# Performance work log

Measured on AMD Instinct MI355X. Metric: run time of the kernel, lower is better.

## Reference

```python
import jax, jax.numpy as jnp
import numpy as np

B, S, H, NH = 2, 2048, 1024, 16
HD = H // NH
EPS = 1e-6

def rotate_half(x):
    x1, x2 = jnp.split(x, 2, axis=-1)
    return jnp.concatenate([-x2, x1], axis=-1)

def setup_inputs() -> dict:
    key = jax.random.key(0)
    ks = jax.random.split(key, 4)
    x = jax.random.normal(ks[0], (B, S, H), dtype=jnp.float32)
    # rotary angles
    inv_freq = 1.0 / (10000.0 ** (np.arange(0, HD, 2, dtype=np.float32) / HD))
    t = np.arange(S, dtype=np.float32)
    freqs = np.einsum('s,d->sd', t, inv_freq)
    emb = np.concatenate([freqs, freqs], axis=-1)  # [S, HD]
    cos = jnp.broadcast_to(jnp.cos(emb)[None], (B, S, HD)).astype(jnp.float32)
    sin = jnp.broadcast_to(jnp.sin(emb)[None], (B, S, HD)).astype(jnp.float32)
    attn_mask = jnp.broadcast_to(jnp.tril(jnp.ones((S, S), jnp.float32))[None], (B, S, S))
    W_uvqk = jax.random.normal(ks[1], (4 * H, H), dtype=jnp.float32) * (1.0 / np.sqrt(H))
    b_uvqk = jnp.zeros((4 * H,), jnp.float32)
    gate_w = jnp.ones((H,), jnp.float32)
    W_out = jax.random.normal(ks[2], (H, H), dtype=jnp.float32) * (1.0 / np.sqrt(H))
    b_out = jnp.zeros((H,), jnp.float32)
    return {"x": x, "cos": cos, "sin": sin, "attn_mask": attn_mask,
            "W_uvqk": W_uvqk, "b_uvqk": b_uvqk, "gate_w": gate_w,
            "W_out": W_out, "b_out": b_out}

def reference(x, cos, sin, attn_mask, W_uvqk, b_uvqk, gate_w, W_out, b_out):
    b, s, h = x.shape
    residual = x
    uvqk = jnp.einsum('bsh,oh->bso', x, W_uvqk) + b_uvqk
    u, v, q, k = jnp.split(uvqk, 4, axis=-1)
    u = jax.nn.silu(u)
    q = q.reshape(b, s, NH, HD)
    k = k.reshape(b, s, NH, HD)
    v = v.reshape(b, s, NH, HD)
    c = cos[:, :, None, :]  # [B,S,1,HD] broadcasts over heads
    sn = sin[:, :, None, :]
    q = q * c + rotate_half(q) * sn
    k = k * c + rotate_half(k) * sn
    # [B,NH,S,S] raw scores -> silu (no softmax) -> mask -> AV
    scores = jnp.einsum('bqnd,bknd->bnqk', q, k) / np.sqrt(HD).astype(np.float32)
    attn = jax.nn.silu(scores) * attn_mask[:, None, :, :]
    attn_out = jnp.einsum('bnqk,bknd->bqnd', attn, v).reshape(b, s, h)
    # RMSNorm (fp32) gating
    ao32 = attn_out.astype(jnp.float32)
    var = jnp.mean(ao32 * ao32, axis=-1, keepdims=True)
    normed = (gate_w * (ao32 * jax.lax.rsqrt(var + EPS))).astype(x.dtype)
    gated = normed * u
    out = jnp.einsum('bsh,oh->bso', gated, W_out) + b_out
    return residual + out
```

## Files before the change

### kernel.cpp

```cpp
#include <hip/hip_runtime.h>

typedef __attribute__((ext_vector_type(4))) float f32x4;
typedef __attribute__((ext_vector_type(8))) short short8;

static __device__ __forceinline__ unsigned short f2bf(float f) {
    union { float f; unsigned int u; } v; v.f = f;
    unsigned int r = v.u + 0x7FFFu + ((v.u >> 16) & 1u);
    return (unsigned short)(r >> 16);
}

static __device__ __forceinline__ float bf2f(unsigned short h) {
    union { unsigned int u; float f; } v; v.u = ((unsigned int)h) << 16;
    return v.f;
}

static __device__ __forceinline__ unsigned int cvt_pk_bf16(float lo, float hi) {
    unsigned int r;
    asm("v_cvt_pk_bf16_f32 %0, %1, %2" : "=v"(r) : "v"(lo), "v"(hi));
    return r;
}

static __device__ __forceinline__ void gload16(const void* g, void* l) {
    __builtin_amdgcn_global_load_lds(
        (const __attribute__((address_space(1))) unsigned int*)g,
        (__attribute__((address_space(3))) unsigned int*)l, 16, 0, 0);
}

static __device__ __forceinline__ void block_sync_raw() {
    asm volatile("" ::: "memory");
    __builtin_amdgcn_s_barrier();
    asm volatile("" ::: "memory");
}

__global__ __launch_bounds__(256) void k_convert(
    const float* __restrict__ x, const float* __restrict__ wu, const float* __restrict__ wo,
    unsigned short* __restrict__ xb, unsigned short* __restrict__ wub, unsigned short* __restrict__ wob)
{
    int i = blockIdx.x * 256 + threadIdx.x;
    const float* src; unsigned short* dst; int off;
    if (i < 1048576)       { src = x;  dst = xb;  off = i; }
    else if (i < 2097152)  { src = wu; dst = wub; off = i - 1048576; }
    else                   { src = wo; dst = wob; off = i - 2097152; }
    float4 v = reinterpret_cast<const float4*>(src)[off];
    ushort4 o;
    o.x = f2bf(v.x); o.y = f2bf(v.y); o.z = f2bf(v.z); o.w = f2bf(v.w);
    reinterpret_cast<ushort4*>(dst)[off] = o;
}

__global__ __launch_bounds__(512, 1) void k_gemm0(
    const unsigned short* __restrict__ A, const unsigned short* __restrict__ Bmat,
    const float* __restrict__ bias,
    unsigned short* __restrict__ u_out, unsigned short* __restrict__ q_out,
    unsigned short* __restrict__ k_out, unsigned short* __restrict__ vt_out,
    const float* __restrict__ cosp, const float* __restrict__ sinp)
{
    const int K = 1024;
    constexpr int NT = 16;
    constexpr int ASZ = 256 * 64;
    constexpr int BSZ = 256 * 64;
    __shared__ __align__(16) unsigned short S[2 * (ASZ + BSZ)];
    int tid = threadIdx.x;
    int lane = tid & 63, wid = tid >> 6;
    int lo = lane & 15, q4 = lane >> 4;
    int x7 = lo & 7;
    int wr = wid >> 2, wc = wid & 3;
    int bn = blockIdx.x, bm = blockIdx.y;
    const unsigned short* Abase = A + (size_t)bm * 256 * K;
    const unsigned short* Bbase = Bmat + (size_t)bn * 256 * K;

    auto stage = [&](int bb, int kt) {
        unsigned short* As = S + bb * (ASZ + BSZ);
        unsigned short* Bs = As + ASZ;
#pragma unroll
        for (int j = 0; j < 4; ++j) {
            int ch = tid + j * 512;
            int r = ch >> 3, p = ch & 7;
            gload16(Abase + (size_t)r * K + kt * 64 + (p ^ (r & 7)) * 8, As + ch * 8);
        }
#pragma unroll
        for (int j = 0; j < 4; ++j) {
            int ch = tid + j * 512;
            int r = ch >> 3, p = ch & 7;
            gload16(Bbase + (size_t)r * K + kt * 64 + (p ^ (r & 7)) * 8, Bs + ch * 8);
        }
    };

    f32x4 acc[8][4] = {};
    stage(0, 0);
    int buf = 0;
    for (int kt = 0; kt < NT; ++kt) {
        if (kt + 1 < NT) {
            stage(buf ^ 1, kt + 1);
            asm volatile("s_waitcnt vmcnt(8)" ::: "memory");
        } else {
            asm volatile("s_waitcnt vmcnt(0)" ::: "memory");
        }
        block_sync_raw();
        const unsigned short* As = S + buf * (ASZ + BSZ);
        const unsigned short* Bs = As + ASZ;
#pragma unroll
        for (int kc = 0; kc < 2; ++kc) {
            int cRd = (kc * 4 + q4) ^ x7;
            short8 af[8], bfr[4];
#pragma unroll
            for (int t = 0; t < 8; ++t)
                af[t] = *(const short8*)&As[(wr * 128 + t * 16 + lo) * 64 + cRd * 8];
#pragma unroll
            for (int t = 0; t < 4; ++t)
                bfr[t] = *(const short8*)&Bs[(wc * 64 + t * 16 + lo) * 64 + cRd * 8];
#pragma unroll
            for (int mt = 0; mt < 8; ++mt)
#pragma unroll
                for (int nt = 0; nt < 4; ++nt)
                    acc[mt][nt] = __builtin_amdgcn_mfma_f32_16x16x32_bf16(af[mt], bfr[nt], acc[mt][nt], 0, 0, 0);
        }
        block_sync_raw();
        buf ^= 1;
    }

    int rowb = bm * 256 + wr * 128;
    int colb = bn * 256 + wc * 64;
    int region = bn >> 2;
    if (region == 1) {
        unsigned short* T = S;
#pragma unroll
        for (int mt = 0; mt < 8; ++mt)
#pragma unroll
            for (int nt = 0; nt < 4; ++nt) {
                float bcol = bias[colb + nt * 16 + lo];
                uint2 w;
                w.x = cvt_pk_bf16(acc[mt][nt][0] + bcol, acc[mt][nt][1] + bcol);
                w.y = cvt_pk_bf16(acc[mt][nt][2] + bcol, acc[mt][nt][3] + bcol);
                int c_local = wc * 64 + nt * 16 + lo;
                int schunk = wr * 16 + mt * 2 + (q4 >> 1);
                *(uint2*)((char*)T + c_local * 512 + ((schunk ^ (c_local & 31)) * 16) + (q4 & 1) * 8) = w;
            }
        __syncthreads();
        int c_row = tid >> 1;
        int bchunk = (tid & 1) * 16;
        int c_global = (bn - 4) * 256 + c_row;
        int head = c_global >> 6, d = c_global & 63;
        int batch = bm >> 3;
        int s_base = (bm * 256) & 2047;
        unsigned short* vrow = vt_out + ((size_t)(batch * 16 + head) * 64 + d) * 2048;
#pragma unroll
        for (int i = 0; i < 16; ++i) {
            int chunk = bchunk + i;
            uint4 v = *(const uint4*)((const char*)T + c_row * 512 + ((chunk ^ (c_row & 31)) * 16));
            *(uint4*)&vrow[s_base + chunk * 8] = v;
        }
    } else {
#pragma unroll
        for (int mt = 0; mt < 8; ++mt) {
#pragma unroll
            for (int r = 0; r < 4; ++r) {
                int rg = rowb + mt * 16 + q4 * 4 + r;
                int b = rg >> 11, s = rg & 2047;
                float vals[4];
#pragma unroll
                for (int nt = 0; nt < 4; ++nt)
                    vals[nt] = acc[mt][nt][r] + bias[colb + nt * 16 + lo];
                if (region == 0) {
#pragma unroll
                    for (int nt = 0; nt < 4; ++nt) {
                        float vv = vals[nt];
                        u_out[(size_t)rg * 1024 + colb + nt * 16 + lo] = f2bf(vv / (1.f + __expf(-vv)));
                    }
                } else {
                    const float* cb = cosp + (size_t)(b * 2048 + s) * 64;
                    const float* sb = sinp + (size_t)(b * 2048 + s) * 64;
                    float o[4];
#pragma unroll
                    for (int nt = 0; nt < 4; ++nt) {
                        int hd = nt * 16 + lo;
                        float partner = (nt < 2) ? -vals[nt + 2] : vals[nt - 2];
                        o[nt] = vals[nt] * cb[hd] + partner * sb[hd];
                    }
                    int c0 = colb - ((region == 2) ? 2048 : 3072);
                    unsigned short* dst = (region == 2) ? q_out : k_out;
#pragma unroll
                    for (int nt = 0; nt < 4; ++nt) {
                        int c = c0 + nt * 16 + lo;
                        int head = c >> 6, d = c & 63;
                        dst[((size_t)(b * 16 + head) * 2048 + s) * 64 + d] = f2bf(o[nt]);
                    }
                }
            }
        }
    }
}

__global__ __launch_bounds__(256) void k_gemm1(
    const unsigned short* __restrict__ A, const unsigned short* __restrict__ Bmat,
    const float* __restrict__ bias, const float* __restrict__ resid, float* __restrict__ out)
{
    const int K = 1024;
    constexpr int NT = 16;
    constexpr int ASZ = 64 * 64;
    constexpr int BSZ = 128 * 64;
    __shared__ __align__(16) unsigned short S[2 * (ASZ + BSZ)];
    int tid = threadIdx.x;
    int lane = tid & 63, wid = tid >> 6;
    int lo = lane & 15, q4 = lane >> 4;
    int x7 = lo & 7;
    int wr = wid >> 1, wc = wid & 1;
    int bn = blockIdx.x, bm = blockIdx.y;
    const unsigned short* Abase = A + (size_t)bm * 64 * K;
    const unsigned short* Bbase = Bmat + (size_t)bn * 128 * K;

    auto stage = [&](int bb, int kt) {
        unsigned short* As = S + bb * (ASZ + BSZ);
        unsigned short* Bs = As + ASZ;
#pragma unroll
        for (int j = 0; j < 2; ++j) {
            int ch = tid + j * 256;
            int r = ch >> 3, p = ch & 7;
            gload16(Abase + (size_t)r * K + kt * 64 + (p ^ (r & 7)) * 8, As + ch * 8);
        }
#pragma unroll
        for (int j = 0; j < 4; ++j) {
            int ch = tid + j * 256;
            int r = ch >> 3, p = ch & 7;
            gload16(Bbase + (size_t)r * K + kt * 64 + (p ^ (r & 7)) * 8, Bs + ch * 8);
        }
    };

    f32x4 acc[2][4] = {};
    stage(0, 0);
    int buf = 0;
    for (int kt = 0; kt < NT; ++kt) {
        if (kt + 1 < NT) {
            stage(buf ^ 1, kt + 1);
            asm volatile("s_waitcnt vmcnt(6)" ::: "memory");
        } else {
            asm volatile("s_waitcnt vmcnt(0)" ::: "memory");
        }
        block_sync_raw();
        const unsigned short* As = S + buf * (ASZ + BSZ);
        const unsigned short* Bs = As + ASZ;
#pragma unroll
        for (int kc = 0; kc < 2; ++kc) {
            int cRd = (kc * 4 + q4) ^ x7;
            short8 af[2], bfr[4];
#pragma unroll
            for (int t = 0; t < 2; ++t)
                af[t] = *(const short8*)&As[(wr * 32 + t * 16 + lo) * 64 + cRd * 8];
#pragma unroll
            for (int t = 0; t < 4; ++t)
                bfr[t] = *(const short8*)&Bs[(wc * 64 + t * 16 + lo) * 64 + cRd * 8];
#pragma unroll
            for (int mt = 0; mt < 2; ++mt)
#pragma unroll
                for (int nt = 0; nt < 4; ++nt)
                    acc[mt][nt] = __builtin_amdgcn_mfma_f32_16x16x32_bf16(af[mt], bfr[nt], acc[mt][nt], 0, 0, 0);
        }
        block_sync_raw();
        buf ^= 1;
    }

    int rowb = bm * 64 + wr * 32;
    int colb = bn * 128 + wc * 64;
#pragma unroll
    for (int mt = 0; mt < 2; ++mt)
#pragma unroll
        for (int r = 0; r < 4; ++r) {
            int rg = rowb + mt * 16 + q4 * 4 + r;
#pragma unroll
            for (int nt = 0; nt < 4; ++nt) {
                int c = colb + nt * 16 + lo;
                out[(size_t)rg * 1024 + c] = acc[mt][nt][r] + bias[c] + resid[(size_t)rg * 1024 + c];
            }
        }
}

__global__ __launch_bounds__(256) void k_attn(
    const unsigned short* __restrict__ Q, const unsigned short* __restrict__ Kg,
    const unsigned short* __restrict__ Vt_g, float* __restrict__ AO0, float* __restrict__ AO1)
{
    __shared__ __align__(16) unsigned short Ksb[2][64 * 64];
    __shared__ __align__(16) unsigned short Vsb[2][64 * 64];
    __shared__ __align__(16) unsigned short Ps[4 * 2048];
    int tid = threadIdx.x;
    int lane = tid & 63, wid = tid >> 6;
    int lo = lane & 15, q4 = lane >> 4;
    int bid = blockIdx.x;
    int bh = bid & 31;
    int s  = bid >> 5;
    int b = bh >> 4, head = bh & 15;

    const unsigned short* Qb = Q    + (size_t)bh * 2048 * 64;
    const unsigned short* Kb = Kg   + (size_t)bh * 2048 * 64;
    const unsigned short* Vb = Vt_g + (size_t)bh * 64 * 2048;
    unsigned short* Pw = Ps + wid * 2048;

    int i0 = wid * 128 + lane;
    int i1 = wid * 128 + 64 + lane;
    int c_0 = i0 & 7, r_0 = i0 >> 3;
    int c_1 = i1 & 7, r_1 = i1 >> 3;
    int cs0 = c_0 ^ (r_0 & 7), cs1 = c_1 ^ (r_1 & 7);
    size_t kOff0 = (size_t)r_0 * 64 + cs0 * 8,  kOff1 = (size_t)r_1 * 64 + cs1 * 8;
    size_t vOff0 = (size_t)r_0 * 2048 + cs0 * 8, vOff1 = (size_t)r_1 * 2048 + cs1 * 8;

    int x7 = lo & 7, qr_rel = q4 >> 1;
    char* pw0 = (char*)Pw + (lo)      * 128 + (q4 & 1) * 8;
    char* pw1 = (char*)Pw + (lo + 16) * 128 + (q4 & 1) * 8;
    int swz[8];
#pragma unroll
    for (int cc = 0; cc < 8; ++cc) swz[cc] = (cc ^ x7) * 16;
    const short8* prd[2][2];
#pragma unroll
    for (int kc = 0; kc < 2; ++kc) {
        prd[0][kc] = (const short8*)&Pw[(lo) * 64      + (((kc * 4 + q4) ^ x7) * 8)];
        prd[1][kc] = (const short8*)&Pw[(16 + lo) * 64 + (((kc * 4 + q4) ^ x7) * 8)];
    }

    auto stage = [&](int bb, int kt) {
        gload16(Kb + (size_t)kt * 4096 + kOff0, &Ksb[bb][i0 * 8]);
        gload16(Kb + (size_t)kt * 4096 + kOff1, &Ksb[bb][i1 * 8]);
        gload16(Vb + (size_t)kt * 64 + vOff0, &Vsb[bb][i0 * 8]);
        gload16(Vb + (size_t)kt * 64 + vOff1, &Vsb[bb][i1 * 8]);
    };

    int J = s;
    int q0w = J * 128 + wid * 32;
    short8 qf[2][2];
#pragma unroll
    for (int qt = 0; qt < 2; ++qt)
#pragma unroll
        for (int kc = 0; kc < 2; ++kc)
            qf[qt][kc] = *(const short8*)(Qb + (size_t)(q0w + qt * 16 + lo) * 64 + kc * 32 + q4 * 8);

    f32x4 oacc[2][4] = {};
    stage(0, 0);
    __syncthreads();
    int buf = 0;

    for (int t = 0; t < 17; ++t) {
        int kt = (t <= s) ? t : (t + 15 - 2 * s);
        if (t < 16) {
            int tn = t + 1;
            int ktn = (tn <= s) ? tn : (tn + 15 - 2 * s);
            stage(buf ^ 1, ktn);
        }
        if (64 * kt <= q0w + 31) {
            f32x4 sacc[4][2] = {};
#pragma unroll
            for (int kc = 0; kc < 2; ++kc)
#pragma unroll
                for (int kt4 = 0; kt4 < 4; ++kt4) {
                    short8 kf = *(const short8*)&Ksb[buf][(kt4 * 16 + lo) * 64 + (((kc * 4 + q4) ^ x7) * 8)];
#pragma unroll
                    for (int qt = 0; qt < 2; ++qt)
                        sacc[kt4][qt] = __builtin_amdgcn_mfma_f32_16x16x32_bf16(kf, qf[qt][kc], sacc[kt4][qt], 0, 0, 0);
                }
            bool needMask = (64 * kt + 63 > q0w);
#pragma unroll
            for (int kt4 = 0; kt4 < 4; ++kt4)
#pragma unroll
                for (int qt = 0; qt < 2; ++qt) {
                    int qc = qt * 16 + lo;
                    float p[4];
#pragma unroll
                    for (int rr = 0; rr < 4; ++rr) {
                        float S = sacc[kt4][qt][rr];
                        float e = __builtin_amdgcn_exp2f(S * -0.180336880f);
                        float pv = S * 0.125f * __builtin_amdgcn_rcpf(1.f + e);
                        if (needMask) {
                            int ky = kt * 64 + kt4 * 16 + q4 * 4 + rr;
                            if (ky > q0w + qc) pv = 0.f;
                        }
                        p[rr] = pv;
                    }
                    uint2 w;
                    w.x = cvt_pk_bf16(p[0], p[1]);
                    w.y = cvt_pk_bf16(p[2], p[3]);
                    *(uint2*)(((qt == 0) ? pw0 : pw1) + swz[kt4 * 2 + qr_rel]) = w;
                }
#pragma unroll
            for (int kc = 0; kc < 2; ++kc) {
                short8 pf0 = *prd[0][kc];
                short8 pf1 = *prd[1][kc];
#pragma unroll
                for (int nt = 0; nt < 4; ++nt) {
                    short8 vf = *(const short8*)&Vsb[buf][(nt * 16 + lo) * 64 + (((kc * 4 + q4) ^ x7) * 8)];
                    oacc[0][nt] = __builtin_amdgcn_mfma_f32_16x16x32_bf16(pf0, vf, oacc[0][nt], 0, 0, 0);
                    oacc[1][nt] = __builtin_amdgcn_mfma_f32_16x16x32_bf16(pf1, vf, oacc[1][nt], 0, 0, 0);
                }
            }
        }
        if (t == s) {
            float* aoLane = AO0 + ((size_t)(b * 2048 + q0w + q4 * 4)) * 1024 + head * 64 + lo;
#pragma unroll
            for (int qt = 0; qt < 2; ++qt)
#pragma unroll
                for (int nt = 0; nt < 4; ++nt)
#pragma unroll
                    for (int rr = 0; rr < 4; ++rr) {
                        aoLane[(qt * 16 + rr) * 1024 + nt * 16] = oacc[qt][nt][rr];
                        oacc[qt][nt][rr] = 0.f;
                    }
            J = 15 - s;
            q0w = J * 128 + wid * 32;
#pragma unroll
            for (int qt = 0; qt < 2; ++qt)
#pragma unroll
                for (int kc = 0; kc < 2; ++kc)
                    qf[qt][kc] = *(const short8*)(Qb + (size_t)(q0w + qt * 16 + lo) * 64 + kc * 32 + q4 * 8);
        }
        __syncthreads();
        buf ^= 1;
    }
    float* aoLane = AO1 + ((size_t)(b * 2048 + q0w + q4 * 4)) * 1024 + head * 64 + lo;
#pragma unroll
    for (int qt = 0; qt < 2; ++qt)
#pragma unroll
        for (int nt = 0; nt < 4; ++nt)
#pragma unroll
            for (int rr = 0; rr < 4; ++rr)
                aoLane[(qt * 16 + rr) * 1024 + nt * 16] = oacc[qt][nt][rr];
}

__global__ __launch_bounds__(256) void k_rmsgate(
    const float* __restrict__ AO0, const float* __restrict__ AO1, const unsigned short* __restrict__ U,
    const float* __restrict__ gw, unsigned short* __restrict__ G)
{
    __shared__ float red[4];
    int row = blockIdx.x, t = threadIdx.x;
    float4 a0 = *(const float4*)&AO0[(size_t)row * 1024 + t * 4];
    float4 a1 = *(const float4*)&AO1[(size_t)row * 1024 + t * 4];
    float4 a;
    a.x = a0.x + a1.x; a.y = a0.y + a1.y; a.z = a0.z + a1.z; a.w = a0.w + a1.w;
    float ss = a.x * a.x + a.y * a.y + a.z * a.z + a.w * a.w;
#pragma unroll
    for (int off = 32; off; off >>= 1) ss += __shfl_down(ss, off);
    int wid = t >> 6, lane = t & 63;
    if (lane == 0) red[wid] = ss;
    __syncthreads();
    float tot = red[0] + red[1] + red[2] + red[3];
    float rs = rsqrtf(tot * (1.f / 1024.f) + 1e-6f);
    float4 g = *(const float4*)&gw[t * 4];
    ushort4 uv = *(const ushort4*)&U[(size_t)row * 1024 + t * 4];
    ushort4 o;
    o.x = f2bf(g.x * a.x * rs * bf2f(uv.x));
    o.y = f2bf(g.y * a.y * rs * bf2f(uv.y));
    o.z = f2bf(g.z * a.z * rs * bf2f(uv.z));
    o.w = f2bf(g.w * a.w * rs * bf2f(uv.w));
    *(ushort4*)&G[(size_t)row * 1024 + t * 4] = o;
}

extern "C" void kernel_launch(void* const* d_in, const int* in_sizes, int n_in,
                              void* d_out, int out_size, void* d_ws, size_t ws_size,
                              hipStream_t stream) {
    const float* x      = (const float*)d_in[0];
    const float* cosp   = (const float*)d_in[1];
    const float* sinp   = (const float*)d_in[2];
    const float* b_uvqk = (const float*)d_in[5];
    const float* gate_w = (const float*)d_in[6];
    const float* b_out  = (const float*)d_in[8];
    float* out = (float*)d_out;

    char* ws = (char*)d_ws;
    unsigned short* xb  = (unsigned short*)(ws);
    unsigned short* wub = (unsigned short*)(ws + 8388608);
    unsigned short* wob = (unsigned short*)(ws + 16777216);
    unsigned short* ub  = (unsigned short*)(ws + 18874368);
    unsigned short* qb  = (unsigned short*)(ws + 35651584);
    unsigned short* kb  = (unsigned short*)(ws + 44040192);
    unsigned short* vtb = (unsigned short*)(ws + 52428800);
    float*          aob = (float*)(ws + 60817408);
    unsigned short* gb  = (unsigned short*)(ws + 77594624);
    float*          ao1 = (float*)(ws);

    k_convert<<<9216, 256, 0, stream>>>((const float*)d_in[0], (const float*)d_in[4],
                                        (const float*)d_in[7], xb, wub, wob);
    k_gemm0<<<dim3(16, 16), 512, 0, stream>>>(xb, wub, b_uvqk, ub, qb, kb, vtb, cosp, sinp);
    k_attn<<<512, 256, 0, stream>>>(qb, kb, vtb, aob, ao1);
    k_rmsgate<<<4096, 256, 0, stream>>>(aob, ao1, ub, gate_w, gb);
    k_gemm1<<<dim3(8, 64), 256, 0, stream>>>(gb, wob, b_out, x, out);
}
```

Measured before the change: 122.1 us.

## Shrink QKV GEMM tiles to 128x128 and store attention partials in bf16

The first GEMM moves from 256x256 tiles with 512 threads to 128x128 tiles with 256 threads on a 32x32 grid. That gives 1024 blocks instead of 256, spreading work more evenly over the CUs and allowing more than one block per CU. The attention kernel now writes its two partial outputs as bf16 instead of fp32, which halves that write traffic and the matching reads in the RMS-gate kernel. The price is lower operand reuse per tile in the GEMM and extra rounding error on the partial sums before they are added and normalized.

```diff
diff --git a/kernel.cpp b/kernel.cpp
--- a/kernel.cpp
+++ b/kernel.cpp
@@ -47,7 +47,7 @@
     reinterpret_cast<ushort4*>(dst)[off] = o;
 }
 
-__global__ __launch_bounds__(512, 1) void k_gemm0(
+__global__ __launch_bounds__(256) void k_gemm0(
     const unsigned short* __restrict__ A, const unsigned short* __restrict__ Bmat,
     const float* __restrict__ bias,
     unsigned short* __restrict__ u_out, unsigned short* __restrict__ q_out,
@@ -56,36 +56,36 @@
 {
     const int K = 1024;
     constexpr int NT = 16;
-    constexpr int ASZ = 256 * 64;
-    constexpr int BSZ = 256 * 64;
+    constexpr int ASZ = 128 * 64;
+    constexpr int BSZ = 128 * 64;
     __shared__ __align__(16) unsigned short S[2 * (ASZ + BSZ)];
     int tid = threadIdx.x;
     int lane = tid & 63, wid = tid >> 6;
     int lo = lane & 15, q4 = lane >> 4;
     int x7 = lo & 7;
-    int wr = wid >> 2, wc = wid & 3;
+    int wr = wid >> 1, wc = wid & 1;
     int bn = blockIdx.x, bm = blockIdx.y;
-    const unsigned short* Abase = A + (size_t)bm * 256 * K;
-    const unsigned short* Bbase = Bmat + (size_t)bn * 256 * K;
+    const unsigned short* Abase = A + (size_t)bm * 128 * K;
+    const unsigned short* Bbase = Bmat + (size_t)bn * 128 * K;
 
     auto stage = [&](int bb, int kt) {
         unsigned short* As = S + bb * (ASZ + BSZ);
         unsigned short* Bs = As + ASZ;
 #pragma unroll
         for (int j = 0; j < 4; ++j) {
-            int ch = tid + j * 512;
+            int ch = tid + j * 256;
             int r = ch >> 3, p = ch & 7;
             gload16(Abase + (size_t)r * K + kt * 64 + (p ^ (r & 7)) * 8, As + ch * 8);
         }
 #pragma unroll
         for (int j = 0; j < 4; ++j) {
-            int ch = tid + j * 512;
+            int ch = tid + j * 256;
             int r = ch >> 3, p = ch & 7;
             gload16(Bbase + (size_t)r * K + kt * 64 + (p ^ (r & 7)) * 8, Bs + ch * 8);
         }
     };
 
-    f32x4 acc[8][4] = {};
+    f32x4 acc[4][4] = {};
     stage(0, 0);
     int buf = 0;
     for (int kt = 0; kt < NT; ++kt) {
@@ -101,15 +101,15 @@
 #pragma unroll
         for (int kc = 0; kc < 2; ++kc) {
             int cRd = (kc * 4 + q4) ^ x7;
-            short8 af[8], bfr[4];
-#pragma unroll
-            for (int t = 0; t < 8; ++t)
-                af[t] = *(const short8*)&As[(wr * 128 + t * 16 + lo) * 64 + cRd * 8];
+            short8 af[4], bfr[4];
+#pragma unroll
+            for (int t = 0; t < 4; ++t)
+                af[t] = *(const short8*)&As[(wr * 64 + t * 16 + lo) * 64 + cRd * 8];
 #pragma unroll
             for (int t = 0; t < 4; ++t)
                 bfr[t] = *(const short8*)&Bs[(wc * 64 + t * 16 + lo) * 64 + cRd * 8];
 #pragma unroll
-            for (int mt = 0; mt < 8; ++mt)
+            for (int mt = 0; mt < 4; ++mt)
 #pragma unroll
                 for (int nt = 0; nt < 4; ++nt)
                     acc[mt][nt] = __builtin_amdgcn_mfma_f32_16x16x32_bf16(af[mt], bfr[nt], acc[mt][nt], 0, 0, 0);
@@ -118,13 +118,13 @@
         buf ^= 1;
     }
 
-    int rowb = bm * 256 + wr * 128;
-    int colb = bn * 256 + wc * 64;
-    int region = bn >> 2;
+    int rowb = bm * 128 + wr * 64;
+    int colb = bn * 128 + wc * 64;
+    int region = bn >> 3;
     if (region == 1) {
         unsigned short* T = S;
 #pragma unroll
-        for (int mt = 0; mt < 8; ++mt)
+        for (int mt = 0; mt < 4; ++mt)
 #pragma unroll
             for (int nt = 0; nt < 4; ++nt) {
                 float bcol = bias[colb + nt * 16 + lo];
@@ -132,26 +132,26 @@
                 w.x = cvt_pk_bf16(acc[mt][nt][0] + bcol, acc[mt][nt][1] + bcol);
                 w.y = cvt_pk_bf16(acc[mt][nt][2] + bcol, acc[mt][nt][3] + bcol);
                 int c_local = wc * 64 + nt * 16 + lo;
-                int schunk = wr * 16 + mt * 2 + (q4 >> 1);
-                *(uint2*)((char*)T + c_local * 512 + ((schunk ^ (c_local & 31)) * 16) + (q4 & 1) * 8) = w;
+                int schunk = wr * 8 + mt * 2 + (q4 >> 1);
+                *(uint2*)((char*)T + c_local * 256 + ((schunk ^ (c_local & 15)) * 16) + (q4 & 1) * 8) = w;
             }
         __syncthreads();
         int c_row = tid >> 1;
-        int bchunk = (tid & 1) * 16;
-        int c_global = (bn - 4) * 256 + c_row;
+        int bchunk = (tid & 1) * 8;
+        int c_global = (bn - 8) * 128 + c_row;
         int head = c_global >> 6, d = c_global & 63;
-        int batch = bm >> 3;
-        int s_base = (bm * 256) & 2047;
+        int batch = (bm * 128) >> 11;
         unsigned short* vrow = vt_out + ((size_t)(batch * 16 + head) * 64 + d) * 2048;
 #pragma unroll
-        for (int i = 0; i < 16; ++i) {
+        for (int i = 0; i < 8; ++i) {
             int chunk = bchunk + i;
-            uint4 v = *(const uint4*)((const char*)T + c_row * 512 + ((chunk ^ (c_row & 31)) * 16));
-            *(uint4*)&vrow[s_base + chunk * 8] = v;
+            uint4 v = *(const uint4*)((const char*)T + c_row * 256 + ((chunk ^ (c_row & 15)) * 16));
+            int s = (bm * 128 + chunk * 8) & 2047;
+            *(uint4*)&vrow[s] = v;
         }
     } else {
 #pragma unroll
-        for (int mt = 0; mt < 8; ++mt) {
+        for (int mt = 0; mt < 4; ++mt) {
 #pragma unroll
             for (int r = 0; r < 4; ++r) {
                 int rg = rowb + mt * 16 + q4 * 4 + r;
@@ -275,7 +275,8 @@
 
 __global__ __launch_bounds__(256) void k_attn(
     const unsigned short* __restrict__ Q, const unsigned short* __restrict__ Kg,
-    const unsigned short* __restrict__ Vt_g, float* __restrict__ AO0, float* __restrict__ AO1)
+    const unsigned short* __restrict__ Vt_g, unsigned short* __restrict__ AO0,
+    unsigned short* __restrict__ AO1)
 {
     __shared__ __align__(16) unsigned short Ksb[2][64 * 64];
     __shared__ __align__(16) unsigned short Vsb[2][64 * 64];
@@ -389,14 +390,14 @@
             }
         }
         if (t == s) {
-            float* aoLane = AO0 + ((size_t)(b * 2048 + q0w + q4 * 4)) * 1024 + head * 64 + lo;
+            unsigned short* aoLane = AO0 + ((size_t)(b * 2048 + q0w + q4 * 4)) * 1024 + head * 64 + lo;
 #pragma unroll
             for (int qt = 0; qt < 2; ++qt)
 #pragma unroll
                 for (int nt = 0; nt < 4; ++nt)
 #pragma unroll
                     for (int rr = 0; rr < 4; ++rr) {
-                        aoLane[(qt * 16 + rr) * 1024 + nt * 16] = oacc[qt][nt][rr];
+                        aoLane[(qt * 16 + rr) * 1024 + nt * 16] = f2bf(oacc[qt][nt][rr]);
                         oacc[qt][nt][rr] = 0.f;
                     }
             J = 15 - s;
@@ -410,26 +411,30 @@
         __syncthreads();
         buf ^= 1;
     }
-    float* aoLane = AO1 + ((size_t)(b * 2048 + q0w + q4 * 4)) * 1024 + head * 64 + lo;
+    unsigned short* aoLane = AO1 + ((size_t)(b * 2048 + q0w + q4 * 4)) * 1024 + head * 64 + lo;
 #pragma unroll
     for (int qt = 0; qt < 2; ++qt)
 #pragma unroll
         for (int nt = 0; nt < 4; ++nt)
 #pragma unroll
             for (int rr = 0; rr < 4; ++rr)
-                aoLane[(qt * 16 + rr) * 1024 + nt * 16] = oacc[qt][nt][rr];
+                aoLane[(qt * 16 + rr) * 1024 + nt * 16] = f2bf(oacc[qt][nt][rr]);
 }
 
 __global__ __launch_bounds__(256) void k_rmsgate(
-    const float* __restrict__ AO0, const float* __restrict__ AO1, const unsigned short* __restrict__ U,
+    const unsigned short* __restrict__ AO0, const unsigned short* __restrict__ AO1,
+    const unsigned short* __restrict__ U,
     const float* __restrict__ gw, unsigned short* __restrict__ G)
 {
     __shared__ float red[4];
     int row = blockIdx.x, t = threadIdx.x;
-    float4 a0 = *(const float4*)&AO0[(size_t)row * 1024 + t * 4];
-    float4 a1 = *(const float4*)&AO1[(size_t)row * 1024 + t * 4];
+    ushort4 a0v = *(const ushort4*)&AO0[(size_t)row * 1024 + t * 4];
+    ushort4 a1v = *(const ushort4*)&AO1[(size_t)row * 1024 + t * 4];
     float4 a;
-    a.x = a0.x + a1.x; a.y = a0.y + a1.y; a.z = a0.z + a1.z; a.w = a0.w + a1.w;
+    a.x = bf2f(a0v.x) + bf2f(a1v.x);
+    a.y = bf2f(a0v.y) + bf2f(a1v.y);
+    a.z = bf2f(a0v.z) + bf2f(a1v.z);
+    a.w = bf2f(a0v.w) + bf2f(a1v.w);
     float ss = a.x * a.x + a.y * a.y + a.z * a.z + a.w * a.w;
 #pragma unroll
     for (int off = 32; off; off >>= 1) ss += __shfl_down(ss, off);
@@ -467,13 +472,13 @@
     unsigned short* qb  = (unsigned short*)(ws + 35651584);
     unsigned short* kb  = (unsigned short*)(ws + 44040192);
     unsigned short* vtb = (unsigned short*)(ws + 52428800);
-    float*          aob = (float*)(ws + 60817408);
+    unsigned short* aob = (unsigned short*)(ws + 60817408);
     unsigned short* gb  = (unsigned short*)(ws + 77594624);
-    float*          ao1 = (float*)(ws);
+    unsigned short* ao1 = (unsigned short*)(ws);
 
     k_convert<<<9216, 256, 0, stream>>>((const float*)d_in[0], (const float*)d_in[4],
                                         (const float*)d_in[7], xb, wub, wob);
-    k_gemm0<<<dim3(16, 16), 512, 0, stream>>>(xb, wub, b_uvqk, ub, qb, kb, vtb, cosp, sinp);
+    k_gemm0<<<dim3(32, 32), 256, 0, stream>>>(xb, wub, b_uvqk, ub, qb, kb, vtb, cosp, sinp);
     k_attn<<<512, 256, 0, stream>>>(qb, kb, vtb, aob, ao1);
     k_rmsgate<<<4096, 256, 0, stream>>>(aob, ao1, ub, gate_w, gb);
     k_gemm1<<<dim3(8, 64), 256, 0, stream>>>(gb, wob, b_out, x, out);
```

Measured after the change: 124.4 us. No clear change (+1.9%).

## Interleave GEMM0 tile loads with MFMA phases and store attention output as bf16

Applied to the files above, without the earlier changes.

The QKV/U projection GEMM main loop now issues the next tile's loads in four groups, one per compute phase, instead of all at once. Each phase is bracketed by barriers and raised wave priority, with staged vmcnt waits, so global-to-LDS traffic overlaps the MFMA work. Separately, the two partial attention outputs are written as bf16 instead of fp32, which halves the traffic written by the attention kernel and read by the RMS-gate kernel. This costs precision on the partial sums before normalization and adds more barriers per K-tile.

```diff
diff --git a/kernel.cpp b/kernel.cpp
--- a/kernel.cpp
+++ b/kernel.cpp
@@ -68,53 +68,61 @@
     const unsigned short* Abase = A + (size_t)bm * 256 * K;
     const unsigned short* Bbase = Bmat + (size_t)bn * 256 * K;
 
-    auto stage = [&](int bb, int kt) {
+    auto stage_group = [&](int bb, int kt, int g) {
         unsigned short* As = S + bb * (ASZ + BSZ);
         unsigned short* Bs = As + ASZ;
-#pragma unroll
-        for (int j = 0; j < 4; ++j) {
-            int ch = tid + j * 512;
-            int r = ch >> 3, p = ch & 7;
-            gload16(Abase + (size_t)r * K + kt * 64 + (p ^ (r & 7)) * 8, As + ch * 8);
-        }
-#pragma unroll
-        for (int j = 0; j < 4; ++j) {
-            int ch = tid + j * 512;
-            int r = ch >> 3, p = ch & 7;
-            gload16(Bbase + (size_t)r * K + kt * 64 + (p ^ (r & 7)) * 8, Bs + ch * 8);
+        if (g < 2) {
+            int i0 = tid, i1 = tid + 512;
+            int r0 = g * 128 + (i0 >> 3), p0 = i0 & 7;
+            int r1 = g * 128 + (i1 >> 3), p1 = i1 & 7;
+            gload16(Bbase + (size_t)r0 * K + kt * 64 + ((p0 ^ (r0 & 7)) * 8), Bs + r0 * 64 + p0 * 8);
+            gload16(Bbase + (size_t)r1 * K + kt * 64 + ((p1 ^ (r1 & 7)) * 8), Bs + r1 * 64 + p1 * 8);
+        } else {
+            int base0 = (g == 2) ? 0 : 64;
+            int r0 = base0 + (tid >> 3), p0 = tid & 7;
+            int r1 = base0 + 128 + (tid >> 3), p1 = tid & 7;
+            gload16(Abase + (size_t)r0 * K + kt * 64 + ((p0 ^ (r0 & 7)) * 8), As + r0 * 64 + p0 * 8);
+            gload16(Abase + (size_t)r1 * K + kt * 64 + ((p1 ^ (r1 & 7)) * 8), As + r1 * 64 + p1 * 8);
         }
     };
 
     f32x4 acc[8][4] = {};
-    stage(0, 0);
+    stage_group(0, 0, 0); stage_group(0, 0, 1); stage_group(0, 0, 2); stage_group(0, 0, 3);
+    asm volatile("s_waitcnt vmcnt(2)" ::: "memory");
+    block_sync_raw();
+
     int buf = 0;
-    for (int kt = 0; kt < NT; ++kt) {
-        if (kt + 1 < NT) {
-            stage(buf ^ 1, kt + 1);
-            asm volatile("s_waitcnt vmcnt(8)" ::: "memory");
-        } else {
-            asm volatile("s_waitcnt vmcnt(0)" ::: "memory");
-        }
-        block_sync_raw();
+    for (int t = 0; t < NT; ++t) {
         const unsigned short* As = S + buf * (ASZ + BSZ);
         const unsigned short* Bs = As + ASZ;
-#pragma unroll
-        for (int kc = 0; kc < 2; ++kc) {
+        bool pre = (t + 1 < NT);
+#pragma unroll
+        for (int p = 0; p < 4; ++p) {
+            const int mh = p >> 1, kc = p & 1;
+            if (pre) stage_group(buf ^ 1, t + 1, p);
             int cRd = (kc * 4 + q4) ^ x7;
-            short8 af[8], bfr[4];
-#pragma unroll
-            for (int t = 0; t < 8; ++t)
-                af[t] = *(const short8*)&As[(wr * 128 + t * 16 + lo) * 64 + cRd * 8];
-#pragma unroll
-            for (int t = 0; t < 4; ++t)
-                bfr[t] = *(const short8*)&Bs[(wc * 64 + t * 16 + lo) * 64 + cRd * 8];
-#pragma unroll
-            for (int mt = 0; mt < 8; ++mt)
-#pragma unroll
-                for (int nt = 0; nt < 4; ++nt)
-                    acc[mt][nt] = __builtin_amdgcn_mfma_f32_16x16x32_bf16(af[mt], bfr[nt], acc[mt][nt], 0, 0, 0);
-        }
-        block_sync_raw();
+            short8 af[4], bfr[4];
+#pragma unroll
+            for (int i = 0; i < 4; ++i)
+                af[i] = *(const short8*)&As[(wr * 128 + mh * 64 + i * 16 + lo) * 64 + cRd * 8];
+#pragma unroll
+            for (int i = 0; i < 4; ++i)
+                bfr[i] = *(const short8*)&Bs[(wc * 64 + i * 16 + lo) * 64 + cRd * 8];
+            block_sync_raw();
+            __builtin_amdgcn_s_setprio(1);
+#pragma unroll
+            for (int i = 0; i < 4; ++i)
+#pragma unroll
+                for (int n = 0; n < 4; ++n)
+                    acc[mh * 4 + i][n] = __builtin_amdgcn_mfma_f32_16x16x32_bf16(af[i], bfr[n], acc[mh * 4 + i][n], 0, 0, 0);
+            __builtin_amdgcn_s_setprio(0);
+            if (p == 1) { asm volatile("s_waitcnt vmcnt(4)" ::: "memory"); }
+            if (p == 3 && pre) {
+                if (t == NT - 2) { asm volatile("s_waitcnt vmcnt(0)" ::: "memory"); }
+                else             { asm volatile("s_waitcnt vmcnt(2)" ::: "memory"); }
+            }
+            block_sync_raw();
+        }
         buf ^= 1;
     }
 
@@ -275,7 +283,8 @@
 
 __global__ __launch_bounds__(256) void k_attn(
     const unsigned short* __restrict__ Q, const unsigned short* __restrict__ Kg,
-    const unsigned short* __restrict__ Vt_g, float* __restrict__ AO0, float* __restrict__ AO1)
+    const unsigned short* __restrict__ Vt_g, unsigned short* __restrict__ AO0,
+    unsigned short* __restrict__ AO1)
 {
     __shared__ __align__(16) unsigned short Ksb[2][64 * 64];
     __shared__ __align__(16) unsigned short Vsb[2][64 * 64];
@@ -389,14 +398,14 @@
             }
         }
         if (t == s) {
-            float* aoLane = AO0 + ((size_t)(b * 2048 + q0w + q4 * 4)) * 1024 + head * 64 + lo;
+            unsigned short* aoLane = AO0 + ((size_t)(b * 2048 + q0w + q4 * 4)) * 1024 + head * 64 + lo;
 #pragma unroll
             for (int qt = 0; qt < 2; ++qt)
 #pragma unroll
                 for (int nt = 0; nt < 4; ++nt)
 #pragma unroll
                     for (int rr = 0; rr < 4; ++rr) {
-                        aoLane[(qt * 16 + rr) * 1024 + nt * 16] = oacc[qt][nt][rr];
+                        aoLane[(qt * 16 + rr) * 1024 + nt * 16] = f2bf(oacc[qt][nt][rr]);
                         oacc[qt][nt][rr] = 0.f;
                     }
             J = 15 - s;
@@ -410,26 +419,30 @@
         __syncthreads();
         buf ^= 1;
     }
-    float* aoLane = AO1 + ((size_t)(b * 2048 + q0w + q4 * 4)) * 1024 + head * 64 + lo;
+    unsigned short* aoLane = AO1 + ((size_t)(b * 2048 + q0w + q4 * 4)) * 1024 + head * 64 + lo;
 #pragma unroll
     for (int qt = 0; qt < 2; ++qt)
 #pragma unroll
         for (int nt = 0; nt < 4; ++nt)
 #pragma unroll
             for (int rr = 0; rr < 4; ++rr)
-                aoLane[(qt * 16 + rr) * 1024 + nt * 16] = oacc[qt][nt][rr];
+                aoLane[(qt * 16 + rr) * 1024 + nt * 16] = f2bf(oacc[qt][nt][rr]);
 }
 
 __global__ __launch_bounds__(256) void k_rmsgate(
-    const float* __restrict__ AO0, const float* __restrict__ AO1, const unsigned short* __restrict__ U,
+    const unsigned short* __restrict__ AO0, const unsigned short* __restrict__ AO1,
+    const unsigned short* __restrict__ U,
     const float* __restrict__ gw, unsigned short* __restrict__ G)
 {
     __shared__ float red[4];
     int row = blockIdx.x, t = threadIdx.x;
-    float4 a0 = *(const float4*)&AO0[(size_t)row * 1024 + t * 4];
-    float4 a1 = *(const float4*)&AO1[(size_t)row * 1024 + t * 4];
+    ushort4 a0v = *(const ushort4*)&AO0[(size_t)row * 1024 + t * 4];
+    ushort4 a1v = *(const ushort4*)&AO1[(size_t)row * 1024 + t * 4];
     float4 a;
-    a.x = a0.x + a1.x; a.y = a0.y + a1.y; a.z = a0.z + a1.z; a.w = a0.w + a1.w;
+    a.x = bf2f(a0v.x) + bf2f(a1v.x);
+    a.y = bf2f(a0v.y) + bf2f(a1v.y);
+    a.z = bf2f(a0v.z) + bf2f(a1v.z);
+    a.w = bf2f(a0v.w) + bf2f(a1v.w);
     float ss = a.x * a.x + a.y * a.y + a.z * a.z + a.w * a.w;
 #pragma unroll
     for (int off = 32; off; off >>= 1) ss += __shfl_down(ss, off);
@@ -467,9 +480,9 @@
     unsigned short* qb  = (unsigned short*)(ws + 35651584);
     unsigned short* kb  = (unsigned short*)(ws + 44040192);
     unsigned short* vtb = (unsigned short*)(ws + 52428800);
-    float*          aob = (float*)(ws + 60817408);
+    unsigned short* aob = (unsigned short*)(ws + 60817408);
     unsigned short* gb  = (unsigned short*)(ws + 77594624);
-    float*          ao1 = (float*)(ws);
+    unsigned short* ao1 = (unsigned short*)(ws);
 
     k_convert<<<9216, 256, 0, stream>>>((const float*)d_in[0], (const float*)d_in[4],
                                         (const float*)d_in[7], xb, wub, wob);
```

After: 119.0 us. -2.5%, faster.
